# Kernel optimization log

Hardware: AMD Instinct MI355X
Metric: run time of the kernel (lower is better)

Reference implementation:

```python
import jax, jax.numpy as jnp
import numpy as np

D, H, O, E, N = 1024, 2048, 1024, 8, 4096

def setup_inputs() -> dict:
    key = jax.random.key(0)
    ks = jax.random.split(key, 5)
    scale = lambda fan_in: 1.0 / np.sqrt(fan_in)
    x = jax.random.normal(ks[0], (N, D), dtype=jnp.float32)
    Wr = jax.random.normal(ks[1], (E, D), dtype=jnp.float32) * scale(D)
    br = jnp.zeros((E,), dtype=jnp.float32)
    W1 = jax.random.normal(ks[2], (E, H, D), dtype=jnp.float32) * scale(D)
    b1 = jnp.zeros((E, H), dtype=jnp.float32)
    W2 = jax.random.normal(ks[3], (E, O, H), dtype=jnp.float32) * scale(H)
    b2 = jnp.zeros((E, O), dtype=jnp.float32)
    return {"x": x, "Wr": Wr, "br": br, "W1": W1, "b1": b1, "W2": W2, "b2": b2}

def reference(x, Wr, br, W1, b1, W2, b2):
    # router softmax over experts: [N, E]
    route = jax.nn.softmax(x @ Wr.T + br, axis=-1)
    # all experts as one grouped GEMM: hidden [N, E, H]
    h = jnp.einsum('nd,ehd->neh', x, W1) + b1
    h = jnp.square(jax.nn.relu(h))  # squared ReLU
    # expert outputs [N, E, O]
    y = jnp.einsum('neh,eoh->neo', h, W2) + b2
    # softmax-weighted combine over experts -> [N, O]
    return jnp.einsum('ne,neo->no', route, y)
```

## Files before the change

kernel.cpp:

```cpp
#include <hip/hip_runtime.h>
#include <hip/hip_bf16.h>
#include <stdint.h>

#define Dd 1024
#define Hd 2048
#define Od 1024
#define Ed 8
#define Nd 4096

typedef __bf16 bf16x8 __attribute__((ext_vector_type(8)));
typedef float f32x4 __attribute__((ext_vector_type(4)));
typedef int i32x4 __attribute__((ext_vector_type(4)));

__device__ __forceinline__ void gload16(const void* g, void* l) {
  __builtin_amdgcn_global_load_lds(
      (const __attribute__((address_space(1))) void*)g,
      (__attribute__((address_space(3))) void*)l, 16, 0, 0);
}

__device__ __forceinline__ unsigned short f2bf(float f) {
  __hip_bfloat16 h = __float2bfloat16(f);
  return *reinterpret_cast<unsigned short*>(&h);
}

__device__ __forceinline__ float blockMax256(float v) {
  __shared__ float sm[4];
  #pragma unroll
  for (int o = 32; o > 0; o >>= 1) v = fmaxf(v, __shfl_down(v, o));
  const int lane = threadIdx.x & 63, w = threadIdx.x >> 6;
  if (lane == 0) sm[w] = v;
  __syncthreads();
  return fmaxf(fmaxf(sm[0], sm[1]), fmaxf(sm[2], sm[3]));
}

template <int K>
__global__ void qrow_kernel(const float* __restrict__ in,
                            signed char* __restrict__ out,
                            float* __restrict__ scale) {
  const int row = blockIdx.x;
  const int t = threadIdx.x;
  const float* r = in + (size_t)row * K;
  float v[K / 256];
  float m = 0.f;
  #pragma unroll
  for (int i = 0; i < K / 256; ++i) {
    v[i] = r[t + i * 256];
    m = fmaxf(m, fabsf(v[i]));
  }
  const float M = blockMax256(m);
  const float inv = (M > 0.f) ? 127.f / M : 0.f;
  signed char* o = out + (size_t)row * K;
  #pragma unroll
  for (int i = 0; i < K / 256; ++i)
    o[t + i * 256] = (signed char)__float2int_rn(v[i] * inv);
  if (t == 0) scale[row] = M / 127.f;
}

__global__ void cvt_kernel(const float* __restrict__ in,
                           unsigned short* __restrict__ out, int ngroups) {
  int stride = gridDim.x * blockDim.x;
  for (int g = blockIdx.x * blockDim.x + threadIdx.x; g < ngroups; g += stride) {
    const float4* p = (const float4*)(in + (size_t)g * 8);
    float4 a = p[0], b = p[1];
    unsigned short o[8];
    o[0] = f2bf(a.x); o[1] = f2bf(a.y); o[2] = f2bf(a.z); o[3] = f2bf(a.w);
    o[4] = f2bf(b.x); o[5] = f2bf(b.y); o[6] = f2bf(b.z); o[7] = f2bf(b.w);
    *(int4*)(out + (size_t)g * 8) = *(int4*)o;
  }
}

__global__ void router_kernel(const float* __restrict__ x, const float* __restrict__ Wr,
                              const float* __restrict__ br, float* __restrict__ route) {
  const int n = blockIdx.x;
  const int t = threadIdx.x;
  __shared__ float xs[Dd];
  float4 v = *(const float4*)&x[(size_t)n * Dd + t * 4];
  *(float4*)&xs[t * 4] = v;
  __syncthreads();
  float p[Ed];
  #pragma unroll
  for (int e = 0; e < Ed; ++e) p[e] = 0.f;
  for (int d = t; d < Dd; d += 256) {
    float xv = xs[d];
    #pragma unroll
    for (int e = 0; e < Ed; ++e) p[e] += xv * Wr[e * Dd + d];
  }
  __shared__ float red[Ed][4];
  const int lane = t & 63, wid = t >> 6;
  #pragma unroll
  for (int e = 0; e < Ed; ++e) {
    float vv = p[e];
    for (int off = 32; off > 0; off >>= 1) vv += __shfl_down(vv, off);
    if (lane == 0) red[e][wid] = vv;
  }
  __syncthreads();
  if (t == 0) {
    float lg[Ed], mx = -1e30f;
    #pragma unroll
    for (int e = 0; e < Ed; ++e) {
      lg[e] = red[e][0] + red[e][1] + red[e][2] + red[e][3] + br[e];
      mx = fmaxf(mx, lg[e]);
    }
    float s = 0.f;
    #pragma unroll
    for (int e = 0; e < Ed; ++e) { lg[e] = expf(lg[e] - mx); s += lg[e]; }
    float inv = 1.f / s;
    #pragma unroll
    for (int e = 0; e < Ed; ++e) route[(size_t)n * Ed + e] = lg[e] * inv;
  }
}

__global__ void init_out_kernel(const float* __restrict__ route, const float* __restrict__ b2,
                                float* __restrict__ out) {
  const int idx = blockIdx.x * 256 + threadIdx.x;
  const int n = idx >> 10, o = idx & (Od - 1);
  float s = 0.f;
  #pragma unroll
  for (int e = 0; e < Ed; ++e) s += route[(size_t)n * Ed + e] * b2[e * Od + o];
  out[idx] = s;
}

__global__ __launch_bounds__(512, 2) void gemmq1(
    const signed char* __restrict__ Ag,
    const signed char* __restrict__ Bg,
    const float* __restrict__ bias,
    const float* __restrict__ route,
    const float* __restrict__ sA,
    const float* __restrict__ sB,
    unsigned short* __restrict__ hs,
    int n0, int ncRows, int ngx) {
  extern __shared__ char smem[];
  char* As = smem;
  char* Bs = smem + 65536;

  const int nwg = gridDim.x;
  const int orig = blockIdx.x;
  const int q8 = nwg >> 3;
  const int wg = (orig & 7) * q8 + (orig >> 3);
  const int bx = wg % ngx;
  const int rem = wg / ngx;
  const int by = rem & 7, ez = rem >> 3;

  const int tid = threadIdx.x;
  const int wid = tid >> 6, lane = tid & 63;
  const int wm = wid >> 2, wn = wid & 3;

  const int KB = Dd;
  const int NT = KB / 128;

  const signed char* Abase = Ag + (size_t)(n0 + bx * 256) * Dd;
  const signed char* Bbase = Bg + (size_t)ez * Hd * Dd + (size_t)(by * 256) * Dd;

  const int trow = tid >> 3;
  const int tcs = ((tid & 7) ^ (trow & 7)) * 16;

  auto stageA = [&](int buf, int kt, int mh) {
    #pragma unroll
    for (int s = 0; s < 2; ++s) {
      const int pa = mh * 128 + s * 64 + trow;
      const int m = ((pa >> 6) & 1) * 128 + ((pa >> 7) & 1) * 64 + (pa & 63);
      gload16(Abase + (size_t)m * KB + kt * 128 + tcs,
              &As[buf * 32768 + (mh * 128 + s * 64) * 128 + wid * 1024]);
    }
  };
  auto stageB = [&](int buf, int kt, int nh) {
    #pragma unroll
    for (int s = 0; s < 2; ++s) {
      const int pb = nh * 128 + s * 64 + trow;
      const int n = ((pb >> 5) & 3) * 64 + ((pb >> 7) & 1) * 32 + (pb & 31);
      gload16(Bbase + (size_t)n * KB + kt * 128 + tcs,
              &Bs[buf * 32768 + (nh * 128 + s * 64) * 128 + wid * 1024]);
    }
  };

  const int laneRow = lane & 15;
  const int swz[2] = { ((lane >> 4) ^ (lane & 7)) * 16,
                       ((4 + (lane >> 4)) ^ (lane & 7)) * 16 };
  const int aRowB = (wm * 64 + laneRow) * 128;
  const int bRowB = (wn * 32 + laneRow) * 128;

  auto rdA = [&](int buf, int mh, int mi, int kk) -> i32x4 {
    return *(const i32x4*)(As + buf * 32768 + aRowB + (mh * 128 + mi * 16) * 128 + swz[kk]);
  };
  auto rdB = [&](int buf, int nh, int ni, int kk) -> i32x4 {
    return *(const i32x4*)(Bs + buf * 32768 + bRowB + (nh * 128 + ni * 16) * 128 + swz[kk]);
  };

  i32x4 acc[8][4];
  #pragma unroll
  for (int i = 0; i < 8; ++i)
    #pragma unroll
    for (int j = 0; j < 4; ++j) acc[i][j] = (i32x4){0, 0, 0, 0};
  i32x4 a0[4][2], a1[4][2], b0[2][2], b1[2][2];

  stageA(0, 0, 0); stageB(0, 0, 0); stageA(0, 0, 1); stageB(0, 0, 1);
  asm volatile("s_waitcnt vmcnt(0)" ::: "memory");
  __builtin_amdgcn_sched_barrier(0);
  __builtin_amdgcn_s_barrier();

  for (int U = 0; U < NT; ++U) {
    const int buf = U & 1;
    if (U + 1 < NT) {
      stageA(buf ^ 1, U + 1, 0); stageB(buf ^ 1, U + 1, 0);
      stageA(buf ^ 1, U + 1, 1); stageB(buf ^ 1, U + 1, 1);
    }
    #pragma unroll
    for (int mi = 0; mi < 4; ++mi) { a0[mi][0] = rdA(buf, 0, mi, 0); a0[mi][1] = rdA(buf, 0, mi, 1); }
    #pragma unroll
    for (int ni = 0; ni < 2; ++ni) { b0[ni][0] = rdB(buf, 0, ni, 0); b0[ni][1] = rdB(buf, 0, ni, 1); }
    __builtin_amdgcn_s_setprio(1);
    #pragma unroll
    for (int kk = 0; kk < 2; ++kk)
      #pragma unroll
      for (int mi = 0; mi < 4; ++mi)
        #pragma unroll
        for (int ni = 0; ni < 2; ++ni)
          acc[mi][ni] = __builtin_amdgcn_mfma_i32_16x16x64_i8(a0[mi][kk], b0[ni][kk], acc[mi][ni], 0, 0, 0);
    __builtin_amdgcn_s_setprio(0);
    #pragma unroll
    for (int mi = 0; mi < 4; ++mi) { a1[mi][0] = rdA(buf, 1, mi, 0); a1[mi][1] = rdA(buf, 1, mi, 1); }
    __builtin_amdgcn_s_setprio(1);
    #pragma unroll
    for (int kk = 0; kk < 2; ++kk)
      #pragma unroll
      for (int mi = 0; mi < 4; ++mi)
        #pragma unroll
        for (int ni = 0; ni < 2; ++ni)
          acc[4 + mi][ni] = __builtin_amdgcn_mfma_i32_16x16x64_i8(a1[mi][kk], b0[ni][kk], acc[4 + mi][ni], 0, 0, 0);
    __builtin_amdgcn_s_setprio(0);
    #pragma unroll
    for (int ni = 0; ni < 2; ++ni) { b1[ni][0] = rdB(buf, 1, ni, 0); b1[ni][1] = rdB(buf, 1, ni, 1); }
    __builtin_amdgcn_s_setprio(1);
    #pragma unroll
    for (int kk = 0; kk < 2; ++kk)
      #pragma unroll
      for (int mi = 0; mi < 4; ++mi)
        #pragma unroll
        for (int ni = 0; ni < 2; ++ni)
          acc[4 + mi][2 + ni] = __builtin_amdgcn_mfma_i32_16x16x64_i8(a1[mi][kk], b1[ni][kk], acc[4 + mi][2 + ni], 0, 0, 0);
    __builtin_amdgcn_s_setprio(0);
    __builtin_amdgcn_s_setprio(1);
    #pragma unroll
    for (int kk = 0; kk < 2; ++kk)
      #pragma unroll
      for (int mi = 0; mi < 4; ++mi)
        #pragma unroll
        for (int ni = 0; ni < 2; ++ni)
          acc[mi][2 + ni] = __builtin_amdgcn_mfma_i32_16x16x64_i8(a0[mi][kk], b1[ni][kk], acc[mi][2 + ni], 0, 0, 0);
    __builtin_amdgcn_s_setprio(0);
    if (U + 1 < NT) {
      asm volatile("s_waitcnt vmcnt(0)" ::: "memory");
    }
    __builtin_amdgcn_sched_barrier(0);
    __builtin_amdgcn_s_barrier();
  }

  unsigned short* base = hs + (size_t)ez * ((size_t)ncRows * Hd);
  #pragma unroll
  for (int M = 0; M < 8; ++M) {
    const int mh = M >> 2, mi = M & 3;
    const int rowc = bx * 256 + wm * 128 + mh * 64 + mi * 16 + (lane >> 4) * 4;
    float sx4[4], rw[4];
    #pragma unroll
    for (int j = 0; j < 4; ++j) {
      sx4[j] = sA[n0 + rowc + j];
      rw[j] = route[(size_t)(n0 + rowc + j) * Ed + ez];
    }
    #pragma unroll
    for (int N = 0; N < 4; ++N) {
      const int nh = N >> 1, ni = N & 1;
      const int col = by * 256 + wn * 64 + nh * 32 + ni * 16 + (lane & 15);
      const float sw = sB[ez * Hd + col];
      const float bv = bias[ez * Hd + col];
      #pragma unroll
      for (int j = 0; j < 4; ++j) {
        float v = (float)acc[M][N][j] * (sx4[j] * sw) + bv;
        v = fmaxf(v, 0.f);
        v = v * v * rw[j];
        base[(size_t)(rowc + j) * Hd + col] = f2bf(v);
      }
    }
  }
}

__global__ __launch_bounds__(512, 2) void gemm2b(
    const unsigned short* __restrict__ Ag,
    const unsigned short* __restrict__ Bg,
    float* __restrict__ out,
    int n0, int ncRows, int ngx) {
  extern __shared__ char smemc[];
  unsigned short* As = (unsigned short*)smemc;
  unsigned short* Bs = (unsigned short*)(smemc + 65536);

  const int nwg = gridDim.x;
  const int orig = blockIdx.x;
  const int q8 = nwg >> 3;
  const int wg = (orig & 7) * q8 + (orig >> 3);
  const int bx = wg % ngx;
  const int rem = wg / ngx;
  const int by = rem & 3, ez = rem >> 2;

  const int tid = threadIdx.x;
  const int wid = tid >> 6, lane = tid & 63;
  const int wm = wid >> 2, wn = wid & 3;

  const int NT = 2 * Hd / 64;

  const int trow = tid >> 3;
  const int tcs = ((tid & 7) ^ (trow & 7)) * 8;

  auto stageA = [&](int buf, int kt, int mh) {
    const int e = ez * 2 + (kt >> 5);
    const size_t Ab = (size_t)e * ncRows * Hd + (size_t)(bx * 256) * Hd;
    const int k0 = (kt & 31) * 64;
    #pragma unroll
    for (int s = 0; s < 2; ++s) {
      const int pa = mh * 128 + s * 64 + trow;
      const int m = ((pa >> 6) & 1) * 128 + ((pa >> 7) & 1) * 64 + (pa & 63);
      gload16(Ag + Ab + (size_t)m * Hd + k0 + tcs,
              &As[(size_t)buf * 16384 + (size_t)(mh * 128 + s * 64) * 64 + wid * 512]);
    }
  };
  auto stageB = [&](int buf, int kt, int nh) {
    const int e = ez * 2 + (kt >> 5);
    const size_t Bb = (size_t)e * Od * Hd + (size_t)(by * 256) * Hd;
    const int k0 = (kt & 31) * 64;
    #pragma unroll
    for (int s = 0; s < 2; ++s) {
      const int pb = nh * 128 + s * 64 + trow;
      const int n = ((pb >> 5) & 3) * 64 + ((pb >> 7) & 1) * 32 + (pb & 31);
      gload16(Bg + Bb + (size_t)n * Hd + k0 + tcs,
              &Bs[(size_t)buf * 16384 + (size_t)(nh * 128 + s * 64) * 64 + wid * 512]);
    }
  };

  const int laneRow = lane & 15;
  const int swzc[2] = { ((lane >> 4) ^ (lane & 7)) << 3,
                        (((lane >> 4) + 4) ^ (lane & 7)) << 3 };
  const int aRowBase = (wm * 64 + laneRow) * 64;
  const int bRowBase = (wn * 32 + laneRow) * 64;

  auto rdA = [&](int buf, int mh, int mi, int kk) -> bf16x8 {
    return *(const bf16x8*)&As[buf * 16384 + aRowBase + (mh * 128 + mi * 16) * 64 + swzc[kk]];
  };
  auto rdB = [&](int buf, int nh, int ni, int kk) -> bf16x8 {
    return *(const bf16x8*)&Bs[buf * 16384 + bRowBase + (nh * 128 + ni * 16) * 64 + swzc[kk]];
  };

  f32x4 acc[8][4];
  #pragma unroll
  for (int i = 0; i < 8; ++i)
    #pragma unroll
    for (int j = 0; j < 4; ++j) acc[i][j] = (f32x4){0.f, 0.f, 0.f, 0.f};
  bf16x8 a0[4][2], a1[4][2], b0[2][2], b1[2][2];

  stageA(0, 0, 0); stageB(0, 0, 0); stageA(0, 0, 1); stageB(0, 0, 1);
  asm volatile("s_waitcnt vmcnt(0)" ::: "memory");
  __builtin_amdgcn_sched_barrier(0);
  __builtin_amdgcn_s_barrier();

  for (int U = 0; U < NT; ++U) {
    const int buf = U & 1;
    if (U + 1 < NT) {
      stageA(buf ^ 1, U + 1, 0); stageB(buf ^ 1, U + 1, 0);
      stageA(buf ^ 1, U + 1, 1); stageB(buf ^ 1, U + 1, 1);
    }
    #pragma unroll
    for (int mi = 0; mi < 4; ++mi) { a0[mi][0] = rdA(buf, 0, mi, 0); a0[mi][1] = rdA(buf, 0, mi, 1); }
    #pragma unroll
    for (int ni = 0; ni < 2; ++ni) { b0[ni][0] = rdB(buf, 0, ni, 0); b0[ni][1] = rdB(buf, 0, ni, 1); }
    __builtin_amdgcn_s_setprio(1);
    #pragma unroll
    for (int kk = 0; kk < 2; ++kk)
      #pragma unroll
      for (int mi = 0; mi < 4; ++mi)
        #pragma unroll
        for (int ni = 0; ni < 2; ++ni)
          acc[mi][ni] = __builtin_amdgcn_mfma_f32_16x16x32_bf16(a0[mi][kk], b0[ni][kk], acc[mi][ni], 0, 0, 0);
    __builtin_amdgcn_s_setprio(0);
    #pragma unroll
    for (int mi = 0; mi < 4; ++mi) { a1[mi][0] = rdA(buf, 1, mi, 0); a1[mi][1] = rdA(buf, 1, mi, 1); }
    __builtin_amdgcn_s_setprio(1);
    #pragma unroll
    for (int kk = 0; kk < 2; ++kk)
      #pragma unroll
      for (int mi = 0; mi < 4; ++mi)
        #pragma unroll
        for (int ni = 0; ni < 2; ++ni)
          acc[4 + mi][ni] = __builtin_amdgcn_mfma_f32_16x16x32_bf16(a1[mi][kk], b0[ni][kk], acc[4 + mi][ni], 0, 0, 0);
    __builtin_amdgcn_s_setprio(0);
    #pragma unroll
    for (int ni = 0; ni < 2; ++ni) { b1[ni][0] = rdB(buf, 1, ni, 0); b1[ni][1] = rdB(buf, 1, ni, 1); }
    __builtin_amdgcn_s_setprio(1);
    #pragma unroll
    for (int kk = 0; kk < 2; ++kk)
      #pragma unroll
      for (int mi = 0; mi < 4; ++mi)
        #pragma unroll
        for (int ni = 0; ni < 2; ++ni)
          acc[4 + mi][2 + ni] = __builtin_amdgcn_mfma_f32_16x16x32_bf16(a1[mi][kk], b1[ni][kk], acc[4 + mi][2 + ni], 0, 0, 0);
    __builtin_amdgcn_s_setprio(0);
    __builtin_amdgcn_s_setprio(1);
    #pragma unroll
    for (int kk = 0; kk < 2; ++kk)
      #pragma unroll
      for (int mi = 0; mi < 4; ++mi)
        #pragma unroll
        for (int ni = 0; ni < 2; ++ni)
          acc[mi][2 + ni] = __builtin_amdgcn_mfma_f32_16x16x32_bf16(a0[mi][kk], b1[ni][kk], acc[mi][2 + ni], 0, 0, 0);
    __builtin_amdgcn_s_setprio(0);
    if (U + 1 < NT) {
      asm volatile("s_waitcnt vmcnt(0)" ::: "memory");
    }
    __builtin_amdgcn_sched_barrier(0);
    __builtin_amdgcn_s_barrier();
  }

  #pragma unroll
  for (int M = 0; M < 8; ++M) {
    const int mh = M >> 2, mi = M & 3;
    const int row = n0 + bx * 256 + wm * 128 + mh * 64 + mi * 16 + (lane >> 4) * 4;
    #pragma unroll
    for (int N = 0; N < 4; ++N) {
      const int nh = N >> 1, ni = N & 1;
      const int col = by * 256 + wn * 64 + nh * 32 + ni * 16 + (lane & 15);
      #pragma unroll
      for (int j = 0; j < 4; ++j)
        atomicAdd(out + (size_t)(row + j) * Od + col, acc[M][N][j]);
    }
  }
}

extern "C" void kernel_launch(void* const* d_in, const int* in_sizes, int n_in,
                              void* d_out, int out_size, void* d_ws, size_t ws_size,
                              hipStream_t stream) {
  const float* x  = (const float*)d_in[0];
  const float* Wr = (const float*)d_in[1];
  const float* br = (const float*)d_in[2];
  const float* W1 = (const float*)d_in[3];
  const float* b1 = (const float*)d_in[4];
  const float* W2 = (const float*)d_in[5];
  const float* b2 = (const float*)d_in[6];
  float* out = (float*)d_out;

  char* ws = (char*)d_ws;
  size_t off = 0;
  auto alloc = [&](size_t bytes) { char* p = ws + off; off += (bytes + 255) & ~255ULL; return p; };
  float* route = (float*)alloc((size_t)Nd * Ed * 4);
  float* sx    = (float*)alloc((size_t)Nd * 4);
  float* sw1   = (float*)alloc((size_t)Ed * Hd * 4);
  signed char* xq  = (signed char*)alloc((size_t)Nd * Dd);
  signed char* w1q = (signed char*)alloc((size_t)Ed * Hd * Dd);
  unsigned short* w2b = (unsigned short*)alloc((size_t)Ed * Od * Hd * 2);
  unsigned short* hs = (unsigned short*)(ws + off);

  size_t remain = (ws_size > off) ? (ws_size - off) : 0;
  const size_t perRow = (size_t)Ed * Hd * 2;
  long long ncMax = (long long)(remain / perRow);
  int NC = (int)(ncMax & ~255LL);
  if (NC > Nd) NC = Nd;
  if (NC < 256) NC = 256;

  hipFuncSetAttribute(reinterpret_cast<const void*>(&gemmq1),
                      hipFuncAttributeMaxDynamicSharedMemorySize, 131072);
  hipFuncSetAttribute(reinterpret_cast<const void*>(&gemm2b),
                      hipFuncAttributeMaxDynamicSharedMemorySize, 131072);

  qrow_kernel<Dd><<<Nd, 256, 0, stream>>>(x, xq, sx);
  qrow_kernel<Dd><<<Ed * Hd, 256, 0, stream>>>(W1, w1q, sw1);
  cvt_kernel<<<2048, 256, 0, stream>>>(W2, w2b, Ed * Od * Hd / 8);
  router_kernel<<<Nd, 256, 0, stream>>>(x, Wr, br, route);
  init_out_kernel<<<Nd * Od / 256, 256, 0, stream>>>(route, b2, out);

  for (int n0 = 0; n0 < Nd; n0 += NC) {
    int nc = (NC < (Nd - n0)) ? NC : (Nd - n0);
    int ngx = nc / 256;
    gemmq1<<<ngx * 8 * Ed, 512, 131072, stream>>>(
        xq, w1q, b1, route, sx, sw1, hs, n0, nc, ngx);
    gemm2b<<<ngx * 4 * 4, 512, 131072, stream>>>(hs, w2b, out, n0, nc, ngx);
  }
}
```

Baseline: 323.0 us.

## Fuse x quantization and output-bias init into router; overlap W2 bf16 convert with GEMM1

The router kernel now also quantizes each x row to int8 with its scale and writes the route-weighted b2 bias into the output, which removes two separate launches and a second read of x. The fp32-to-bf16 conversion of W2 is spread across the gemmq1 blocks of the first chunk, interleaved with the K loop, so its memory traffic can overlap the int8 MFMA work. In exchange, the GEMM main loop gains extra global loads and stores that may compete with its own staging bandwidth and add register pressure.

```diff
diff --git a/kernel.cpp b/kernel.cpp
--- a/kernel.cpp
+++ b/kernel.cpp
@@ -56,27 +56,24 @@
   if (t == 0) scale[row] = M / 127.f;
 }
 
-__global__ void cvt_kernel(const float* __restrict__ in,
-                           unsigned short* __restrict__ out, int ngroups) {
-  int stride = gridDim.x * blockDim.x;
-  for (int g = blockIdx.x * blockDim.x + threadIdx.x; g < ngroups; g += stride) {
-    const float4* p = (const float4*)(in + (size_t)g * 8);
-    float4 a = p[0], b = p[1];
-    unsigned short o[8];
-    o[0] = f2bf(a.x); o[1] = f2bf(a.y); o[2] = f2bf(a.z); o[3] = f2bf(a.w);
-    o[4] = f2bf(b.x); o[5] = f2bf(b.y); o[6] = f2bf(b.z); o[7] = f2bf(b.w);
-    *(int4*)(out + (size_t)g * 8) = *(int4*)o;
-  }
-}
-
 __global__ void router_kernel(const float* __restrict__ x, const float* __restrict__ Wr,
-                              const float* __restrict__ br, float* __restrict__ route) {
+                              const float* __restrict__ br, const float* __restrict__ b2,
+                              float* __restrict__ route,
+                              signed char* __restrict__ xq, float* __restrict__ sx,
+                              float* __restrict__ out) {
   const int n = blockIdx.x;
   const int t = threadIdx.x;
   __shared__ float xs[Dd];
   float4 v = *(const float4*)&x[(size_t)n * Dd + t * 4];
   *(float4*)&xs[t * 4] = v;
-  __syncthreads();
+  float m = fmaxf(fmaxf(fabsf(v.x), fabsf(v.y)), fmaxf(fabsf(v.z), fabsf(v.w)));
+  const float M = blockMax256(m);
+  const float inv = (M > 0.f) ? 127.f / M : 0.f;
+  int q0 = __float2int_rn(v.x * inv) & 255, q1 = __float2int_rn(v.y * inv) & 255;
+  int q2 = __float2int_rn(v.z * inv) & 255, q3 = __float2int_rn(v.w * inv) & 255;
+  *(int*)(xq + (size_t)n * Dd + t * 4) = q0 | (q1 << 8) | (q2 << 16) | (q3 << 24);
+  if (t == 0) sx[n] = M / 127.f;
+
   float p[Ed];
   #pragma unroll
   for (int e = 0; e < Ed; ++e) p[e] = 0.f;
@@ -94,6 +91,7 @@
     if (lane == 0) red[e][wid] = vv;
   }
   __syncthreads();
+  __shared__ float rsm[Ed];
   if (t == 0) {
     float lg[Ed], mx = -1e30f;
     #pragma unroll
@@ -104,20 +102,23 @@
     float s = 0.f;
     #pragma unroll
     for (int e = 0; e < Ed; ++e) { lg[e] = expf(lg[e] - mx); s += lg[e]; }
-    float inv = 1.f / s;
-    #pragma unroll
-    for (int e = 0; e < Ed; ++e) route[(size_t)n * Ed + e] = lg[e] * inv;
-  }
-}
-
-__global__ void init_out_kernel(const float* __restrict__ route, const float* __restrict__ b2,
-                                float* __restrict__ out) {
-  const int idx = blockIdx.x * 256 + threadIdx.x;
-  const int n = idx >> 10, o = idx & (Od - 1);
-  float s = 0.f;
-  #pragma unroll
-  for (int e = 0; e < Ed; ++e) s += route[(size_t)n * Ed + e] * b2[e * Od + o];
-  out[idx] = s;
+    float is = 1.f / s;
+    #pragma unroll
+    for (int e = 0; e < Ed; ++e) {
+      float rv = lg[e] * is;
+      route[(size_t)n * Ed + e] = rv;
+      rsm[e] = rv;
+    }
+  }
+  __syncthreads();
+  float4 acc = {0.f, 0.f, 0.f, 0.f};
+  #pragma unroll
+  for (int e = 0; e < Ed; ++e) {
+    float4 bv = *(const float4*)&b2[e * Od + t * 4];
+    float rv = rsm[e];
+    acc.x += rv * bv.x; acc.y += rv * bv.y; acc.z += rv * bv.z; acc.w += rv * bv.w;
+  }
+  *(float4*)&out[(size_t)n * Od + t * 4] = acc;
 }
 
 __global__ __launch_bounds__(512, 2) void gemmq1(
@@ -128,6 +129,9 @@
     const float* __restrict__ sA,
     const float* __restrict__ sB,
     unsigned short* __restrict__ hs,
+    const float* __restrict__ W2f,
+    unsigned short* __restrict__ w2cv,
+    int cvtGroups,
     int n0, int ncRows, int ngx) {
   extern __shared__ char smem[];
   char* As = smem;
@@ -148,6 +152,11 @@
   const int KB = Dd;
   const int NT = KB / 128;
 
+  const int cvtPerBlk = (cvtGroups + nwg - 1) / nwg;
+  const int cvtBase = orig * cvtPerBlk;
+  const int cvtEnd = (cvtBase + cvtPerBlk < cvtGroups) ? cvtBase + cvtPerBlk : cvtGroups;
+  const int perIter = (cvtPerBlk + NT - 1) / NT;
+
   const signed char* Abase = Ag + (size_t)(n0 + bx * 256) * Dd;
   const signed char* Bbase = Bg + (size_t)ez * Hd * Dd + (size_t)(by * 256) * Dd;
 
@@ -203,6 +212,18 @@
     if (U + 1 < NT) {
       stageA(buf ^ 1, U + 1, 0); stageB(buf ^ 1, U + 1, 0);
       stageA(buf ^ 1, U + 1, 1); stageB(buf ^ 1, U + 1, 1);
+    }
+    for (int r = 0; r < perIter; r += 512) {
+      const int idx = r + tid;
+      const int g = cvtBase + U * perIter + idx;
+      if (idx < perIter && g < cvtEnd) {
+        const float4* p = (const float4*)(W2f + (size_t)g * 8);
+        float4 a = p[0], b = p[1];
+        unsigned short o[8];
+        o[0] = f2bf(a.x); o[1] = f2bf(a.y); o[2] = f2bf(a.z); o[3] = f2bf(a.w);
+        o[4] = f2bf(b.x); o[5] = f2bf(b.y); o[6] = f2bf(b.z); o[7] = f2bf(b.w);
+        *(int4*)(w2cv + (size_t)g * 8) = *(int4*)o;
+      }
     }
     #pragma unroll
     for (int mi = 0; mi < 4; ++mi) { a0[mi][0] = rdA(buf, 0, mi, 0); a0[mi][1] = rdA(buf, 0, mi, 1); }
@@ -466,17 +487,18 @@
   hipFuncSetAttribute(reinterpret_cast<const void*>(&gemm2b),
                       hipFuncAttributeMaxDynamicSharedMemorySize, 131072);
 
-  qrow_kernel<Dd><<<Nd, 256, 0, stream>>>(x, xq, sx);
   qrow_kernel<Dd><<<Ed * Hd, 256, 0, stream>>>(W1, w1q, sw1);
-  cvt_kernel<<<2048, 256, 0, stream>>>(W2, w2b, Ed * Od * Hd / 8);
-  router_kernel<<<Nd, 256, 0, stream>>>(x, Wr, br, route);
-  init_out_kernel<<<Nd * Od / 256, 256, 0, stream>>>(route, b2, out);
-
+  router_kernel<<<Nd, 256, 0, stream>>>(x, Wr, br, b2, route, xq, sx, out);
+
+  const int cvtGroups = Ed * Od * Hd / 8;
+  bool first = true;
   for (int n0 = 0; n0 < Nd; n0 += NC) {
     int nc = (NC < (Nd - n0)) ? NC : (Nd - n0);
     int ngx = nc / 256;
     gemmq1<<<ngx * 8 * Ed, 512, 131072, stream>>>(
-        xq, w1q, b1, route, sx, sw1, hs, n0, nc, ngx);
+        xq, w1q, b1, route, sx, sw1, hs, W2, w2b,
+        first ? cvtGroups : 0, n0, nc, ngx);
+    first = false;
     gemm2b<<<ngx * 4 * 4, 512, 131072, stream>>>(hs, w2b, out, n0, nc, ngx);
   }
 }
```

Result: faster. 297.8 us (-7.8%).
